# Performance work log

Measured on AMD Instinct MI355X. Metric: run time of the kernel, lower is better.

Reference implementation:

```python
import jax, jax.numpy as jnp
import numpy as np

H = 64  # hidden size
I = 300  # input size
NEG_SLOPE = 0.01  # LeakyReLU default


def _gru_scan(x_proj, W_hh, b_hh):
    """x_proj: [T, B, 3H] precomputed input projections (+ b_ih).
    Returns all hidden states [T, B, H] starting from h0 = 0."""
    B = x_proj.shape[1]
    h0 = jnp.zeros((B, H), dtype=x_proj.dtype)

    def step(h, xp):
        gh = h @ W_hh.T + b_hh  # [B, 3H]
        xr, xz, xn = jnp.split(xp, 3, axis=-1)
        hr, hz, hn = jnp.split(gh, 3, axis=-1)
        r = jax.nn.sigmoid(xr + hr)
        z = jax.nn.sigmoid(xz + hz)
        n = jnp.tanh(xn + r * hn)
        h_new = (1.0 - z) * n + z * h
        return h_new, h_new

    _, hs = jax.lax.scan(step, h0, x_proj)
    return hs  # [T, B, H]


def _forward(x, W_ih_f, W_hh_f, b_ih_f, b_hh_f, W_ih_b, W_hh_b, b_ih_b, b_hh_b,
             W1, b1, W2, b2):
    # x: [B, T, I]
    xt = jnp.swapaxes(x, 0, 1)  # [T, B, I]
    xp_f = jnp.einsum('tbi,gi->tbg', xt, W_ih_f) + b_ih_f  # [T, B, 3H]
    xp_b = jnp.einsum('tbi,gi->tbg', xt[::-1], W_ih_b) + b_ih_b

    hs_f = _gru_scan(xp_f, W_hh_f, b_hh_f)            # [T, B, H]
    hs_b = _gru_scan(xp_b, W_hh_b, b_hh_b)[::-1]      # [T, B, H] (realigned)

    out = jnp.concatenate([hs_f, hs_b], axis=-1)      # [T, B, 2H]
    x_first = out[0]    # [B, 2H]
    x_last = out[-1]    # [B, 2H]
    feat = jnp.concatenate([x_first, x_last], axis=1)  # [B, 4H]

    h1 = feat @ W1.T + b1
    h1 = jnp.where(h1 >= 0, h1, NEG_SLOPE * h1)  # LeakyReLU
    return h1 @ W2.T + b2  # [B, 1]


def setup_inputs() -> dict:
    key = jax.random.key(0)
    ks = jax.random.split(key, 16)
    B, T = 256, 512
    s_gru = 1.0 / np.sqrt(H)
    s1 = 1.0 / np.sqrt(256)
    s2 = 1.0 / np.sqrt(32)
    u = lambda k, shape, s: jax.random.uniform(k, shape, jnp.float32, -s, s)
    return {
        'x': jax.random.normal(ks[0], (B, T, I), dtype=jnp.float32),
        'W_ih_f': u(ks[1], (3 * H, I), s_gru),
        'W_hh_f': u(ks[2], (3 * H, H), s_gru),
        'b_ih_f': u(ks[3], (3 * H,), s_gru),
        'b_hh_f': u(ks[4], (3 * H,), s_gru),
        'W_ih_b': u(ks[5], (3 * H, I), s_gru),
        'W_hh_b': u(ks[6], (3 * H, H), s_gru),
        'b_ih_b': u(ks[7], (3 * H,), s_gru),
        'b_hh_b': u(ks[8], (3 * H,), s_gru),
        'W1': u(ks[9], (32, 4 * H), s1),
        'b1': u(ks[10], (32,), s1),
        'W2': u(ks[11], (1, 32), s2),
        'b2': u(ks[12], (1,), s2),
    }


def reference(x, W_ih_f, W_hh_f, b_ih_f, b_hh_f, W_ih_b, W_hh_b, b_ih_b, b_hh_b,
              W1, b1, W2, b2):
    return _forward(x, W_ih_f, W_hh_f, b_ih_f, b_hh_f,
                    W_ih_b, W_hh_b, b_ih_b, b_hh_b, W1, b1, W2, b2)
```

## Files before the change

kernel.cpp:

```cpp
#include <hip/hip_runtime.h>
#include <hip/hip_bf16.h>
#include <math.h>

#define T_LEN 512
#define B_SZ  256
#define I_SZ  300
#define H_SZ  64
#define G3    192
#define TPG   3072
#define HPAD  80

typedef float    f4v __attribute__((ext_vector_type(4)));
typedef _Float16 h4v __attribute__((ext_vector_type(4)));
typedef _Float16 h8v __attribute__((ext_vector_type(8)));

__device__ __forceinline__ float sigm_f(float x) {
    return __builtin_amdgcn_rcpf(1.f + __expf(-x));
}
__device__ __forceinline__ float tanh_f(float x) {
    float a = fabsf(x);
    float e = __expf(2.f * a);
    float t = 1.f - 2.f * __builtin_amdgcn_rcpf(1.f + e);
    return copysignf(t, x);
}

__device__ __forceinline__ void lds_barrier() {
    __builtin_amdgcn_sched_barrier(0);
    asm volatile("s_waitcnt lgkmcnt(0)\n\ts_barrier" ::: "memory");
    __builtin_amdgcn_sched_barrier(0);
}

#define KC  64
#define NKC 5

__device__ __forceinline__ int stage_off(int j, int srow, int skq) {
    int g2 = (skq >> 1) & 3;
    return j * 1024 + (skq >> 3) * 512 + g2 * 128 + ((srow ^ (g2 << 1)) << 3) + (skq & 1) * 4;
}
__device__ __forceinline__ int frag_off(int tile, int kh, int lane) {
    int kgrp = lane >> 4, fr = lane & 15;
    return tile * 1024 + kh * 512 + kgrp * 128 + (((fr ^ (kgrp << 1))) << 3);
}

__global__ __launch_bounds__(256, 2) void proj_gemm(
    const float* __restrict__ x,
    const float* __restrict__ Wf, const float* __restrict__ bf,
    const float* __restrict__ Wb, const float* __restrict__ bb,
    _Float16* __restrict__ xp)
{
    __shared__ _Float16 Ap[8 * 1024];
    __shared__ _Float16 Bp[12 * 1024];

    const int tid = threadIdx.x;
    const int bid = blockIdx.x;
    const int d   = bid >> 10;
    const int G   = (bid >> 6) & 15;
    const int tc  = bid & 63;

    const float* W    = d ? Wb : Wf;
    const float* bias = d ? bb : bf;

    const int srow = tid >> 4;
    const int skq  = tid & 15;

    const int lane = tid & 63;
    const int w    = tid >> 6;
    const int wn   = (w >> 1) * 96;

    f4v acc[4][6];
    #pragma unroll
    for (int mt = 0; mt < 4; ++mt)
        #pragma unroll
        for (int nt = 0; nt < 6; ++nt) acc[mt][nt] = (f4v)0.f;

    float4 av[8], bv[12];
    {
        const bool valid = (skq * 4) <= 296;
        #pragma unroll
        for (int j = 0; j < 8; ++j)
            av[j] = valid ? *(const float4*)(x + ((size_t)(G * 16 + srow) * T_LEN + tc * 8 + j) * I_SZ + skq * 4)
                          : float4{0.f, 0.f, 0.f, 0.f};
        #pragma unroll
        for (int j = 0; j < 12; ++j)
            bv[j] = valid ? *(const float4*)(W + (size_t)(j * 16 + srow) * I_SZ + skq * 4)
                          : float4{0.f, 0.f, 0.f, 0.f};
    }

    for (int kc = 0; kc < NKC; ++kc) {
        __syncthreads();

        #pragma unroll
        for (int j = 0; j < 8; ++j) {
            h4v c = { (_Float16)av[j].x, (_Float16)av[j].y,
                      (_Float16)av[j].z, (_Float16)av[j].w };
            *(h4v*)&Ap[stage_off(j, srow, skq)] = c;
        }
        #pragma unroll
        for (int j = 0; j < 12; ++j) {
            h4v c = { (_Float16)bv[j].x, (_Float16)bv[j].y,
                      (_Float16)bv[j].z, (_Float16)bv[j].w };
            *(h4v*)&Bp[stage_off(j, srow, skq)] = c;
        }
        __syncthreads();

        if (kc + 1 < NKC) {
            const int k0 = (kc + 1) * KC;
            const bool valid = (k0 + skq * 4) <= 296;
            #pragma unroll
            for (int j = 0; j < 8; ++j)
                av[j] = valid ? *(const float4*)(x + ((size_t)(G * 16 + srow) * T_LEN + tc * 8 + j) * I_SZ + k0 + skq * 4)
                              : float4{0.f, 0.f, 0.f, 0.f};
            #pragma unroll
            for (int j = 0; j < 12; ++j)
                bv[j] = valid ? *(const float4*)(W + (size_t)(j * 16 + srow) * I_SZ + k0 + skq * 4)
                              : float4{0.f, 0.f, 0.f, 0.f};
        }

        #pragma unroll
        for (int kh = 0; kh < 2; ++kh) {
            h8v bh_[6];
            #pragma unroll
            for (int nt = 0; nt < 6; ++nt)
                bh_[nt] = *(const h8v*)&Bp[frag_off((w >> 1) * 6 + nt, kh, lane)];
            #pragma unroll
            for (int mt = 0; mt < 4; ++mt) {
                h8v ah = *(const h8v*)&Ap[frag_off((w & 1) * 4 + mt, kh, lane)];
                #pragma unroll
                for (int nt = 0; nt < 6; ++nt)
                    acc[mt][nt] = __builtin_amdgcn_mfma_f32_16x16x32_f16(ah, bh_[nt], acc[mt][nt], 0, 0, 0);
            }
        }
    }

    const int col  = lane & 15;
    const int rowq = lane >> 4;
    float bias_v[6];
    #pragma unroll
    for (int nt = 0; nt < 6; ++nt) bias_v[nt] = bias[wn + nt * 16 + col];

    _Float16* obase = xp + (size_t)(d * 16 + G) * T_LEN * TPG;
    #pragma unroll
    for (int mt = 0; mt < 4; ++mt) {
        int t = tc * 8 + (w & 1) * 4 + mt;
        _Float16* ot = obase + (size_t)t * TPG;
        #pragma unroll
        for (int nt = 0; nt < 6; ++nt) {
            int g = wn + nt * 16 + col;
            float bb_ = bias_v[nt];
            #pragma unroll
            for (int i = 0; i < 4; ++i)
                ot[(rowq * 4 + i) * G3 + g] = (_Float16)(acc[mt][nt][i] + bb_);
        }
    }
}

__global__ __launch_bounds__(256) void gru_scan(
    const _Float16* __restrict__ xp2,
    const float* __restrict__ Whf, const float* __restrict__ bhf,
    const float* __restrict__ Whb, const float* __restrict__ bhb,
    float* __restrict__ feat)
{
    const int tid  = threadIdx.x;
    const int lane = tid & 63;
    const int w    = tid >> 6;
    const int blk  = blockIdx.x;
    const int d    = blk >> 6;
    const int G    = (blk >> 2) & 15;
    const int sub  = blk & 3;
    const int col  = lane & 15;
    const int quad = lane >> 4;
    const int u    = w * 16 + col;
    const int bm   = sub * 4 + quad;

    const float* Whh = d ? Whb : Whf;
    const float* bhh = d ? bhb : bhf;

    h8v wb[3][2];
    f4v accb[3];
    int loff[3];
    #pragma unroll
    for (int g = 0; g < 3; ++g) {
        const int n = g * 64 + u;
        const float* wrow = Whh + (size_t)n * 64;
        #pragma unroll
        for (int c = 0; c < 2; ++c) {
            float4 w0 = *(const float4*)(wrow + c * 32 + quad * 8);
            float4 w1 = *(const float4*)(wrow + c * 32 + quad * 8 + 4);
            wb[g][c] = h8v{(_Float16)w0.x, (_Float16)w0.y, (_Float16)w0.z, (_Float16)w0.w,
                           (_Float16)w1.x, (_Float16)w1.y, (_Float16)w1.z, (_Float16)w1.w};
        }
        float bn = bhh[n];
        accb[g] = f4v{bn, bn, bn, bn};
        loff[g] = bm * G3 + n;
    }

    __shared__ _Float16 hs[2][4 * HPAD];
    for (int i = tid; i < 4 * HPAD; i += 256) hs[0][i] = (_Float16)0.f;
    float hold = 0.f;

    const long tstep = d ? -(long)TPG : (long)TPG;
    const _Float16* base = xp2 + (size_t)(d * 16 + G) * T_LEN * TPG
                               + (size_t)(d ? T_LEN - 1 : 0) * TPG;

    _Float16 px[2][3];
    #pragma unroll
    for (int g = 0; g < 3; ++g) {
        px[0][g] = base[loff[g]];
        px[1][g] = base[tstep + loff[g]];
    }
    const _Float16* pnext = base + 2 * tstep;

    const int off_first = d ? 192 : 0;
    const int off_last  = d ? 64 : 128;

    __syncthreads();

    for (int s = 0; s < T_LEN; s += 2) {
        #pragma unroll
        for (int j = 0; j < 2; ++j) {
            const int sj = s + j;
            const _Float16* hrd = hs[j];
            _Float16*       hwr = hs[j ^ 1];

            h8v a0 = *(const h8v*)&hrd[(col >> 2) * HPAD + quad * 8];
            h8v a1 = *(const h8v*)&hrd[(col >> 2) * HPAD + 32 + quad * 8];

            f4v gh[3];
            #pragma unroll
            for (int g = 0; g < 3; ++g) {
                f4v t0 = __builtin_amdgcn_mfma_f32_16x16x32_f16(a0, wb[g][0], accb[g], 0, 0, 0);
                gh[g]  = __builtin_amdgcn_mfma_f32_16x16x32_f16(a1, wb[g][1], t0, 0, 0, 0);
            }

            _Float16 xc0 = px[j][0], xc1 = px[j][1], xc2 = px[j][2];
            if (sj + 2 < T_LEN) {
                #pragma unroll
                for (int g = 0; g < 3; ++g)
                    px[j][g] = pnext[loff[g]];
                pnext += tstep;
            }

            {
                float r = sigm_f((float)xc0 + gh[0][0]);
                float z = sigm_f((float)xc1 + gh[1][0]);
                float n = tanh_f((float)xc2 + r * gh[2][0]);
                float h = fmaf(z, hold - n, n);
                hold = h;
                hwr[quad * HPAD + u] = (_Float16)h;
            }

            if (sj == 0)
                feat[(G * 16 + bm) * 256 + off_first + u] = hold;
            if (sj == T_LEN - 1)
                feat[(G * 16 + bm) * 256 + off_last + u] = hold;

            lds_barrier();
        }
    }
}

__global__ __launch_bounds__(64) void head_k(
    const float* __restrict__ feat,
    const float* __restrict__ W1, const float* __restrict__ b1,
    const float* __restrict__ W2, const float* __restrict__ b2,
    float* __restrict__ out)
{
    __shared__ float fs[256];
    const int b = blockIdx.x;
    const int tid = threadIdx.x;
    *(float4*)&fs[tid * 4] = *(const float4*)&feat[b * 256 + tid * 4];
    __syncthreads();
    float v = 0.f;
    if (tid < 32) {
        float a = b1[tid];
        const float4* Wv = (const float4*)(W1 + tid * 256);
        const float4* fv = (const float4*)fs;
        #pragma unroll 8
        for (int k = 0; k < 64; ++k) {
            float4 wv = Wv[k], f = fv[k];
            a += wv.x * f.x + wv.y * f.y + wv.z * f.z + wv.w * f.w;
        }
        a = a >= 0.f ? a : 0.01f * a;
        v = a * W2[tid];
    }
    #pragma unroll
    for (int off = 16; off > 0; off >>= 1) v += __shfl_down(v, off);
    if (tid == 0) out[b] = v + b2[0];
}

extern "C" void kernel_launch(void* const* d_in, const int* in_sizes, int n_in,
                              void* d_out, int out_size, void* d_ws, size_t ws_size,
                              hipStream_t stream)
{
    const float* x    = (const float*)d_in[0];
    const float* Wihf = (const float*)d_in[1];
    const float* Whhf = (const float*)d_in[2];
    const float* bihf = (const float*)d_in[3];
    const float* bhhf = (const float*)d_in[4];
    const float* Wihb = (const float*)d_in[5];
    const float* Whhb = (const float*)d_in[6];
    const float* bihb = (const float*)d_in[7];
    const float* bhhb = (const float*)d_in[8];
    const float* W1   = (const float*)d_in[9];
    const float* b1   = (const float*)d_in[10];
    const float* W2   = (const float*)d_in[11];
    const float* b2   = (const float*)d_in[12];
    float* out = (float*)d_out;

    _Float16* xp2  = (_Float16*)d_ws;
    float*    feat = (float*)((char*)d_ws + (size_t)2 * B_SZ * T_LEN * G3 * 2);

    proj_gemm<<<2048, 256, 0, stream>>>(x, Wihf, bihf, Wihb, bihb, xp2);
    gru_scan<<<128, 256, 0, stream>>>(xp2, Whhf, bhhf, Whhb, bhhb, feat);
    head_k<<<256, 64, 0, stream>>>(feat, W1, b1, W2, b2, out);
}
```

Measured before the change: 476.7 us.

## Swap MFMA operand roles in projection GEMM for vectorized fp16 stores

The projection GEMM now puts the weight fragment in the A operand and the input fragment in the B operand, so the accumulator's four consecutive values run along the gate dimension. The epilogue can then write four fp16 values with one 8-byte store instead of four scalar 2-byte stores, and bias is read as a float4. Each wave now handles 2 timesteps across all 12 gate tiles instead of a 4x6 tile split, which changes LDS fragment reuse. The block index mapping is also reordered so the two directions and adjacent time chunks interleave.

```diff
diff --git a/kernel.cpp b/kernel.cpp
--- a/kernel.cpp
+++ b/kernel.cpp
@@ -53,9 +53,9 @@
 
     const int tid = threadIdx.x;
     const int bid = blockIdx.x;
-    const int d   = bid >> 10;
-    const int G   = (bid >> 6) & 15;
-    const int tc  = bid & 63;
+    const int d   = bid & 1;
+    const int tc  = (bid >> 1) & 63;
+    const int G   = bid >> 7;
 
     const float* W    = d ? Wb : Wf;
     const float* bias = d ? bb : bf;
@@ -65,13 +65,12 @@
 
     const int lane = tid & 63;
     const int w    = tid >> 6;
-    const int wn   = (w >> 1) * 96;
-
-    f4v acc[4][6];
-    #pragma unroll
-    for (int mt = 0; mt < 4; ++mt)
-        #pragma unroll
-        for (int nt = 0; nt < 6; ++nt) acc[mt][nt] = (f4v)0.f;
+
+    f4v acc[2][12];
+    #pragma unroll
+    for (int t2 = 0; t2 < 2; ++t2)
+        #pragma unroll
+        for (int gt = 0; gt < 12; ++gt) acc[t2][gt] = (f4v)0.f;
 
     float4 av[8], bv[12];
     {
@@ -118,38 +117,32 @@
 
         #pragma unroll
         for (int kh = 0; kh < 2; ++kh) {
-            h8v bh_[6];
+            h8v xb0 = *(const h8v*)&Ap[frag_off(w * 2 + 0, kh, lane)];
+            h8v xb1 = *(const h8v*)&Ap[frag_off(w * 2 + 1, kh, lane)];
             #pragma unroll
-            for (int nt = 0; nt < 6; ++nt)
-                bh_[nt] = *(const h8v*)&Bp[frag_off((w >> 1) * 6 + nt, kh, lane)];
-            #pragma unroll
-            for (int mt = 0; mt < 4; ++mt) {
-                h8v ah = *(const h8v*)&Ap[frag_off((w & 1) * 4 + mt, kh, lane)];
-                #pragma unroll
-                for (int nt = 0; nt < 6; ++nt)
-                    acc[mt][nt] = __builtin_amdgcn_mfma_f32_16x16x32_f16(ah, bh_[nt], acc[mt][nt], 0, 0, 0);
+            for (int gt = 0; gt < 12; ++gt) {
+                h8v wf = *(const h8v*)&Bp[frag_off(gt, kh, lane)];
+                acc[0][gt] = __builtin_amdgcn_mfma_f32_16x16x32_f16(wf, xb0, acc[0][gt], 0, 0, 0);
+                acc[1][gt] = __builtin_amdgcn_mfma_f32_16x16x32_f16(wf, xb1, acc[1][gt], 0, 0, 0);
             }
         }
     }
 
     const int col  = lane & 15;
     const int rowq = lane >> 4;
-    float bias_v[6];
-    #pragma unroll
-    for (int nt = 0; nt < 6; ++nt) bias_v[nt] = bias[wn + nt * 16 + col];
-
     _Float16* obase = xp + (size_t)(d * 16 + G) * T_LEN * TPG;
     #pragma unroll
-    for (int mt = 0; mt < 4; ++mt) {
-        int t = tc * 8 + (w & 1) * 4 + mt;
+    for (int t2 = 0; t2 < 2; ++t2) {
+        int t = tc * 8 + w * 2 + t2;
         _Float16* ot = obase + (size_t)t * TPG;
         #pragma unroll
-        for (int nt = 0; nt < 6; ++nt) {
-            int g = wn + nt * 16 + col;
-            float bb_ = bias_v[nt];
-            #pragma unroll
-            for (int i = 0; i < 4; ++i)
-                ot[(rowq * 4 + i) * G3 + g] = (_Float16)(acc[mt][nt][i] + bb_);
+        for (int gt = 0; gt < 12; ++gt) {
+            float4 bv4 = *(const float4*)(bias + gt * 16 + rowq * 4);
+            h4v c = { (_Float16)(acc[t2][gt][0] + bv4.x),
+                      (_Float16)(acc[t2][gt][1] + bv4.y),
+                      (_Float16)(acc[t2][gt][2] + bv4.z),
+                      (_Float16)(acc[t2][gt][3] + bv4.w) };
+            *(h4v*)(ot + col * G3 + gt * 16 + rowq * 4) = c;
         }
     }
 }
```

Result: slower. 557.1 us (+16.9%).
